# Performance work log

Measured on AMD Instinct MI355X. Metric: run time of the kernel, lower is better.

Reference implementation:

```python
import jax, jax.numpy as jnp
import numpy as np

AVG_LEN = 60.0
EPS = 1e-5
L, B, C, E = 48, 16, 128, 128
N_AGG = 15  # 5 + 10 * len(['sum'])


def setup_inputs() -> dict:
    key = jax.random.key(0)
    k0, k1, k2, k3 = jax.random.split(key, 4)
    T = jax.random.normal(k0, (L, L, B, C), jnp.float32)
    mask = jax.random.randint(k1, (L, L, B), 0, 2) > 0
    running_mean = jnp.zeros((C,), jnp.float32)
    running_var = jnp.ones((C,), jnp.float32)
    bn_weight = jnp.ones((C,), jnp.float32)
    bn_bias = jnp.zeros((C,), jnp.float32)
    w1 = jax.random.normal(k2, (C, E), jnp.float32) / np.sqrt(C).astype(np.float32)
    b1 = jnp.zeros((E,), jnp.float32)
    w2 = jax.random.normal(k3, (N_AGG * E, C), jnp.float32) / np.sqrt(N_AGG * E).astype(np.float32)
    b2 = jnp.zeros((C,), jnp.float32)
    return dict(T=T, mask=mask, running_mean=running_mean, running_var=running_var,
                bn_weight=bn_weight, bn_bias=bn_bias, w1=w1, b1=b1, w2=w2, b2=b2)


def reference(T, mask, running_mean, running_var, bn_weight, bn_bias, w1, b1, w2, b2):
    n = T.shape[0]
    # MaskedBatchNorm2d, eval mode (running stats)
    Tn = (T - running_mean) / jnp.sqrt(running_var + EPS) * bn_weight + bn_bias
    H = jax.nn.silu(Tn @ w1 + b1)                      # [L, L, B, E]
    eye = jnp.eye(n, dtype=bool)                       # [L, L]
    mf = mask[..., None].astype(H.dtype)               # [L, L, B, 1]
    mdf = (mask & eye[:, :, None])[..., None].astype(H.dtype)
    idx = jnp.arange(n)
    diag = H[idx, idx]                                 # [L, B, E]

    def dembed(x):  # [L, B, E] -> [L, L, B, E] with x on the (0,1)-diagonal
        return jnp.where(eye[:, :, None, None], x[:, None], jnp.zeros((), H.dtype))

    bc = lambda x: jnp.broadcast_to(x, H.shape)
    Hm = H * mf
    row_agg = jnp.sum(Hm, axis=0) / AVG_LEN            # [L, B, E]
    col_agg = jnp.sum(Hm, axis=1) / AVG_LEN            # [L, B, E]
    diag_agg = jnp.sum(H * mdf, axis=(0, 1)) / AVG_LEN # [B, E]
    all_agg = jnp.sum(Hm, axis=(0, 1)) / (AVG_LEN ** 2)  # [B, E]

    parts = [
        dembed(diag), bc(diag[None]), bc(diag[:, None]), jnp.swapaxes(H, 0, 1), H,
        dembed(row_agg), dembed(col_agg),
        dembed(jnp.broadcast_to(diag_agg[None], diag.shape)),
        bc(diag_agg[None, None]), bc(row_agg[None]), bc(col_agg[None]),
        bc(all_agg[None, None]), bc(col_agg[:, None]), bc(row_agg[:, None]),
        bc(all_agg[None, None]),
    ]
    outputs = jnp.concatenate(parts, axis=3)           # [L, L, B, 15*E]
    return outputs @ w2 + b2
```

## Files before the change

### kernel.cpp

```cpp
#include <hip/hip_runtime.h>

typedef __attribute__((ext_vector_type(8))) short short8;
typedef __attribute__((ext_vector_type(4))) float f32x4;
typedef __attribute__((ext_vector_type(4))) unsigned short ushort4_t;

#define NL 48
#define NB 16
#define NROWS (NL*NL*NB)

#define HB_N     (NROWS*128/2)
#define HB_OFF   0
#define W1T_OFF  (HB_OFF + HB_N)
#define W34T_OFF (W1T_OFF + 8192)
#define WD_OFF   (W34T_OFF + 16384)
#define X2_OFF   (WD_OFF + 73728)
#define VEC_N    (NL*NB*128)
#define RA_OFF   (X2_OFF + 147456)
#define AJ_OFF   (RA_OFF + VEC_N)
#define AI_OFF   (AJ_OFF + VEC_N)
#define AD_OFF   (AI_OFF + VEC_N)
#define AB_OFF   (AD_OFF + VEC_N)
#define DGA_OFF  (AB_OFF + NB*128)
#define FLAG_OFF (DGA_OFF + NB*128)

__device__ __forceinline__ float silu_f(float x) { return x / (1.0f + __expf(-x)); }
__device__ __forceinline__ unsigned short f2bf(float x) {
  union { float f; unsigned u; } v; v.f = x;
  unsigned r = v.u + 0x7fffu + ((v.u >> 16) & 1u);
  return (unsigned short)(r >> 16);
}
__device__ __forceinline__ float bf2f(unsigned short h) {
  union { unsigned u; float f; } v; v.u = ((unsigned)h) << 16; return v.f;
}

__global__ __launch_bounds__(256) void kPrep(const float* __restrict__ w1,
    const float* __restrict__ w2, const unsigned char* __restrict__ mb,
    unsigned short* __restrict__ w1t, unsigned short* __restrict__ w34t,
    unsigned short* __restrict__ wd, int* __restrict__ flag)
{
  __shared__ float t[64*65];
  __shared__ int any;
  int blk = blockIdx.x, tid = threadIdx.x;
  if (blk < 4) {
    int k0 = (blk & 1)*64, n0 = (blk >> 1)*64;
    #pragma unroll
    for (int it = 0; it < 16; ++it) { int f = it*256+tid; int kk=f>>6, nn=f&63;
      t[kk*65+nn] = w1[(k0+kk)*128 + n0+nn]; }
    __syncthreads();
    #pragma unroll
    for (int it = 0; it < 16; ++it) { int f = it*256+tid; int nn=f>>6, kk=f&63;
      w1t[(n0+nn)*128 + k0+kk] = f2bf(t[kk*65+nn]); }
  } else if (blk < 12) {
    int q = blk-4; int k0 = (q&3)*64, n0 = (q>>2)*64;
    #pragma unroll
    for (int it = 0; it < 16; ++it) { int f = it*256+tid; int kk=f>>6, nn=f&63;
      int k = k0+kk; int slice = (k < 128) ? 4 : 3;
      t[kk*65+nn] = w2[slice*16384 + (k&127)*128 + n0+nn]; }
    __syncthreads();
    #pragma unroll
    for (int it = 0; it < 16; ++it) { int f = it*256+tid; int nn=f>>6, kk=f&63;
      w34t[(n0+nn)*256 + k0+kk] = f2bf(t[kk*65+nn]); }
  } else if (blk < 48) {
    int q = blk-12; int k0 = (q%6)*64, n0 = (q/6)*64;
    int nq = n0 >> 7, kq = k0 >> 7;
    int slice;
    {
      const int sl_aj[3] = {1,9,10};
      const int sl_ai[3] = {2,13,12};
      const int sl_ad[3] = {0,5,6};
      slice = (nq==0) ? sl_aj[kq] : (nq==1) ? sl_ai[kq] : sl_ad[kq];
    }
    int nb = n0 & 127;
    #pragma unroll
    for (int it = 0; it < 16; ++it) { int f = it*256+tid; int kk=f>>6, nn=f&63;
      t[kk*65+nn] = w2[slice*16384 + ((k0&127)+kk)*128 + nb+nn]; }
    __syncthreads();
    #pragma unroll
    for (int it = 0; it < 16; ++it) { int f = it*256+tid; int nn=f>>6, kk=f&63;
      wd[(n0+nn)*384 + k0+kk] = f2bf(t[kk*65+nn]); }
  } else {
    if (tid == 0) any = 0;
    __syncthreads();
    int acc = 0;
    #pragma unroll
    for (int k2 = 0; k2 < 12; ++k2) {
      uchar4 v = ((const uchar4*)mb)[tid + k2*256];
      acc |= v.y | v.z | v.w;
    }
    if (acc) atomicOr(&any, 1);
    __syncthreads();
    if (tid == 0) *flag = any ? 1 : 4;
  }
}

__global__ __launch_bounds__(256) void kA(const float* __restrict__ T,
    const float* __restrict__ rmean, const float* __restrict__ rvar,
    const float* __restrict__ bw, const float* __restrict__ bb,
    const unsigned short* __restrict__ w1t, const float* __restrict__ b1,
    unsigned short* __restrict__ Hb)
{
  __shared__ __align__(16) char XDS[64*256];
  __shared__ __align__(16) char WDS[128*256];
  int tid = threadIdx.x;
  int m0 = blockIdx.x * 64;

  int cbase = (tid & 31) * 4;
  float scr[4], shr[4];
  #pragma unroll
  for (int u = 0; u < 4; ++u) {
    float s = bw[cbase+u] * rsqrtf(rvar[cbase+u] + 1e-5f);
    scr[u] = s; shr[u] = bb[cbase+u] - rmean[cbase+u] * s;
  }
  #pragma unroll
  for (int t = 0; t < 8; ++t) {
    int f = t*256 + tid;
    int r = f >> 5, c4 = f & 31;
    float4 v = *(const float4*)&T[(m0 + r)*128 + c4*4];
    ushort4_t p;
    p.x = f2bf(v.x*scr[0] + shr[0]); p.y = f2bf(v.y*scr[1] + shr[1]);
    p.z = f2bf(v.z*scr[2] + shr[2]); p.w = f2bf(v.w*scr[3] + shr[3]);
    *(ushort4_t*)(XDS + r*256 + ((c4*8) ^ ((r & 7) << 4))) = p;
  }
  #pragma unroll
  for (int t = 0; t < 8; ++t) {
    int f = t*256 + tid;
    int r = f >> 4, c16 = f & 15;
    short8 v = *(const short8*)(w1t + r*128 + c16*8);
    *(short8*)(WDS + r*256 + ((c16*16) ^ ((r & 7) << 4))) = v;
  }
  __syncthreads();

  int wave = tid >> 6, lane = tid & 63;
  int ln = lane & 15, lg = lane >> 4;
  int rw = (wave >> 1) * 32, cw = (wave & 1) * 64;
  int swz = (ln & 7) << 4;
  f32x4 acc[2][4];
  #pragma unroll
  for (int mt = 0; mt < 2; ++mt)
    #pragma unroll
    for (int nt = 0; nt < 4; ++nt) acc[mt][nt] = (f32x4){0.f,0.f,0.f,0.f};

  #pragma unroll
  for (int ks = 0; ks < 4; ++ks) {
    int kb = ks*64 + lg*16;
    short8 a[2], b[4];
    #pragma unroll
    for (int mt = 0; mt < 2; ++mt)
      a[mt] = *(const short8*)(XDS + (rw + mt*16 + ln)*256 + (kb ^ swz));
    #pragma unroll
    for (int nt = 0; nt < 4; ++nt)
      b[nt] = *(const short8*)(WDS + (cw + nt*16 + ln)*256 + (kb ^ swz));
    #pragma unroll
    for (int mt = 0; mt < 2; ++mt)
      #pragma unroll
      for (int nt = 0; nt < 4; ++nt)
        acc[mt][nt] = __builtin_amdgcn_mfma_f32_16x16x32_bf16(a[mt], b[nt], acc[mt][nt], 0, 0, 0);
  }
  float b1v[4];
  #pragma unroll
  for (int nt = 0; nt < 4; ++nt) b1v[nt] = b1[cw + nt*16 + ln];
  #pragma unroll
  for (int mt = 0; mt < 2; ++mt)
    #pragma unroll
    for (int q = 0; q < 4; ++q) {
      int m = m0 + rw + mt*16 + 4*lg + q;
      #pragma unroll
      for (int nt = 0; nt < 4; ++nt) {
        float x = acc[mt][nt][q] + b1v[nt];
        Hb[m*128 + cw + nt*16 + ln] = f2bf(silu_f(x));
      }
    }
}

__global__ __launch_bounds__(128) void kAgg(const unsigned short* __restrict__ Hb,
    const unsigned char* __restrict__ mb, const int* __restrict__ flag,
    float* __restrict__ ra, unsigned short* __restrict__ X2)
{
  int p = blockIdx.x, b = blockIdx.y;
  int tid = threadIdx.x;
  int s = *flag;
  int half = tid >> 6;
  int t = tid & 63;
  float a0 = 0.f, a1 = 0.f;
  #pragma unroll 16
  for (int q = 0; q < NL; ++q) {
    int mi = half ? ((q*NL + p)*NB + b) : ((p*NL + q)*NB + b);
    float mv = (float)mb[mi*s];
    unsigned u = *(const unsigned*)(Hb + mi*128 + 2*t);
    a0 += mv * bf2f((unsigned short)(u & 0xffffu));
    a1 += mv * bf2f((unsigned short)(u >> 16));
  }
  a0 *= (1.0f/60.0f); a1 *= (1.0f/60.0f);
  int ix = p*NB + b;
  unsigned pk = ((unsigned)f2bf(a1) << 16) | (unsigned)f2bf(a0);
  if (half) {
    *(float2*)(ra + ix*128 + 2*t) = make_float2(a0, a1);
    *(unsigned*)(X2 + ix*384 + 128 + 2*t) = pk;
  } else {
    *(unsigned*)(X2 + ix*384 + 256 + 2*t) = pk;
    unsigned d = *(const unsigned*)(Hb + ((p*NL + p)*NB + b)*128 + 2*t);
    *(unsigned*)(X2 + ix*384 + 2*t) = d;
  }
}

__global__ __launch_bounds__(256) void kDm(const unsigned short* __restrict__ X2,
    const unsigned short* __restrict__ wd,
    const unsigned short* __restrict__ Hb, const unsigned char* __restrict__ mb,
    const int* __restrict__ flag, const float* __restrict__ ra,
    const float* __restrict__ w2, const float* __restrict__ b2,
    float* __restrict__ Aj, float* __restrict__ Ai, float* __restrict__ Adg,
    float* __restrict__ Ab, float* __restrict__ Dga)
{
  int tid = threadIdx.x;
  if (blockIdx.y == 3) {
    int b = blockIdx.x;
    __shared__ float aas[128], dgs[128];
    int e = tid & 127;
    if (tid < 128) {
      int s = *flag;
      float aa = 0.f, dg = 0.f;
      #pragma unroll 8
      for (int p = 0; p < NL; ++p) {
        aa += ra[(p*NB + b)*128 + e];
        int mi = (p*NL + p)*NB + b;
        dg += (float)mb[mi*s] * bf2f(Hb[mi*128 + e]);
      }
      aas[e] = aa * (1.0f/60.0f);
      dgs[e] = dg * (1.0f/60.0f);
    }
    __syncthreads();
    if (tid < 128) {
      float ab = b2[e];
      #pragma unroll 8
      for (int k = 0; k < 128; ++k) {
        int o = k*128 + e;
        ab += dgs[k]*w2[8*16384 + o] + aas[k]*(w2[11*16384 + o] + w2[14*16384 + o]);
      }
      Ab[b*128 + e] = ab;
    } else {
      float dga = 0.f;
      #pragma unroll 8
      for (int k = 0; k < 128; ++k)
        dga += dgs[k]*w2[7*16384 + k*128 + e];
      Dga[b*128 + e] = dga;
    }
    return;
  }
  if (blockIdx.x >= 12) return;

  __shared__ __align__(16) char ADS[64*256];
  __shared__ __align__(16) char BDS[128*256];
  int m0 = blockIdx.x * 64;
  int n0 = blockIdx.y * 128;

  int wave = tid >> 6, lane = tid & 63;
  int ln = lane & 15, lg = lane >> 4;
  int rw = (wave >> 1) * 32, cw = (wave & 1) * 64;
  int swzk = (ln & 7) << 4;
  f32x4 acc[2][4];
  #pragma unroll
  for (int mt = 0; mt < 2; ++mt)
    #pragma unroll
    for (int nt = 0; nt < 4; ++nt) acc[mt][nt] = (f32x4){0.f,0.f,0.f,0.f};

  for (int kc = 0; kc < 3; ++kc) {
    if (kc) __syncthreads();
    #pragma unroll
    for (int t = 0; t < 4; ++t) {
      int f = t*256 + tid;
      int r = f >> 4, c16 = f & 15;
      short8 v = *(const short8*)(X2 + (m0 + r)*384 + kc*128 + c16*8);
      *(short8*)(ADS + r*256 + ((c16*16) ^ ((r & 7) << 4))) = v;
    }
    #pragma unroll
    for (int t = 0; t < 8; ++t) {
      int f = t*256 + tid;
      int r = f >> 4, c16 = f & 15;
      short8 v = *(const short8*)(wd + (n0 + r)*384 + kc*128 + c16*8);
      *(short8*)(BDS + r*256 + ((c16*16) ^ ((r & 7) << 4))) = v;
    }
    __syncthreads();
    #pragma unroll
    for (int ks = 0; ks < 4; ++ks) {
      int kb = ks*64 + lg*16;
      short8 a[2], b[4];
      #pragma unroll
      for (int mt = 0; mt < 2; ++mt)
        a[mt] = *(const short8*)(ADS + (rw + mt*16 + ln)*256 + (kb ^ swzk));
      #pragma unroll
      for (int nt = 0; nt < 4; ++nt)
        b[nt] = *(const short8*)(BDS + (cw + nt*16 + ln)*256 + (kb ^ swzk));
      #pragma unroll
      for (int mt = 0; mt < 2; ++mt)
        #pragma unroll
        for (int nt = 0; nt < 4; ++nt)
          acc[mt][nt] = __builtin_amdgcn_mfma_f32_16x16x32_bf16(a[mt], b[nt], acc[mt][nt], 0, 0, 0);
    }
  }
  float* outp = (blockIdx.y == 0) ? Aj : (blockIdx.y == 1) ? Ai : Adg;
  #pragma unroll
  for (int mt = 0; mt < 2; ++mt)
    #pragma unroll
    for (int q = 0; q < 4; ++q) {
      int row = m0 + rw + mt*16 + 4*lg + q;
      #pragma unroll
      for (int nt = 0; nt < 4; ++nt)
        outp[row*128 + cw + nt*16 + ln] = acc[mt][nt][q];
    }
}

__global__ __launch_bounds__(256) void kE(const unsigned short* __restrict__ Hb,
    const unsigned short* __restrict__ w34t,
    const float* __restrict__ Aj, const float* __restrict__ Ai,
    const float* __restrict__ Adg, const float* __restrict__ Ab,
    const float* __restrict__ Dga,
    float* __restrict__ out)
{
  __shared__ __align__(16) char ADS[64*512];
  __shared__ __align__(16) char BDS[128*256];
  int tid = threadIdx.x;
  int bi = blockIdx.x / 12;
  int j0 = (blockIdx.x % 12) * 4;

  #pragma unroll
  for (int t = 0; t < 8; ++t) {
    int f = t*256 + tid;
    int r = f >> 5, c16 = f & 31;
    int j = j0 + (r >> 4), b = r & 15;
    int srcrow = (c16 < 16) ? ((bi*NL + j)*NB + b) : ((j*NL + bi)*NB + b);
    short8 v = *(const short8*)(Hb + srcrow*128 + (c16 & 15)*8);
    *(short8*)(ADS + r*512 + ((c16*16) ^ ((r & 7) << 4))) = v;
  }

  int wave = tid >> 6, lane = tid & 63;
  int ln = lane & 15, lg = lane >> 4;
  int rw = (wave >> 1) * 32, cw = (wave & 1) * 64;
  int swz = (ln & 7) << 4;
  f32x4 acc[2][4];
  #pragma unroll
  for (int mt = 0; mt < 2; ++mt)
    #pragma unroll
    for (int nt = 0; nt < 4; ++nt) acc[mt][nt] = (f32x4){0.f,0.f,0.f,0.f};

  #pragma unroll
  for (int half = 0; half < 2; ++half) {
    __syncthreads();
    #pragma unroll
    for (int t = 0; t < 8; ++t) {
      int f = t*256 + tid;
      int r = f >> 4, c16 = f & 15;
      short8 v = *(const short8*)(w34t + r*256 + half*128 + c16*8);
      *(short8*)(BDS + r*256 + ((c16*16) ^ ((r & 7) << 4))) = v;
    }
    __syncthreads();
    #pragma unroll
    for (int ks = 0; ks < 4; ++ks) {
      int kbA = half*256 + ks*64 + lg*16;
      int kbB = ks*64 + lg*16;
      short8 a[2], b[4];
      #pragma unroll
      for (int mt = 0; mt < 2; ++mt)
        a[mt] = *(const short8*)(ADS + (rw + mt*16 + ln)*512 + (kbA ^ swz));
      #pragma unroll
      for (int nt = 0; nt < 4; ++nt)
        b[nt] = *(const short8*)(BDS + (cw + nt*16 + ln)*256 + (kbB ^ swz));
      #pragma unroll
      for (int mt = 0; mt < 2; ++mt)
        #pragma unroll
        for (int nt = 0; nt < 4; ++nt)
          acc[mt][nt] = __builtin_amdgcn_mfma_f32_16x16x32_bf16(a[mt], b[nt], acc[mt][nt], 0, 0, 0);
    }
  }

  #pragma unroll
  for (int mt = 0; mt < 2; ++mt) {
    int tb = rw + mt*16;
    int jj = tb >> 4;
    int j = j0 + jj;
    bool isdiag = (bi == j);
    #pragma unroll
    for (int q = 0; q < 4; ++q) {
      int b = 4*lg + q;
      int m = (bi*NL + j)*NB + b;
      #pragma unroll
      for (int nt = 0; nt < 4; ++nt) {
        int n = cw + nt*16 + ln;
        float add = Aj[(j*NB + b)*128 + n] + Ai[(bi*NB + b)*128 + n] + Ab[b*128 + n];
        if (isdiag) add += Adg[(bi*NB + b)*128 + n] + Dga[b*128 + n];
        out[m*128 + n] = acc[mt][nt][q] + add;
      }
    }
  }
}

extern "C" void kernel_launch(void* const* d_in, const int* in_sizes, int n_in,
                              void* d_out, int out_size, void* d_ws, size_t ws_size,
                              hipStream_t stream) {
  (void)in_sizes; (void)n_in; (void)out_size; (void)ws_size;
  const float* T      = (const float*)d_in[0];
  const unsigned char* mask = (const unsigned char*)d_in[1];
  const float* rmean  = (const float*)d_in[2];
  const float* rvar   = (const float*)d_in[3];
  const float* bw     = (const float*)d_in[4];
  const float* bb     = (const float*)d_in[5];
  const float* w1     = (const float*)d_in[6];
  const float* b1     = (const float*)d_in[7];
  const float* w2     = (const float*)d_in[8];
  const float* b2     = (const float*)d_in[9];
  float* ws  = (float*)d_ws;
  float* out = (float*)d_out;

  unsigned short* Hb   = (unsigned short*)(ws + HB_OFF);
  unsigned short* w1t  = (unsigned short*)(ws + W1T_OFF);
  unsigned short* w34t = (unsigned short*)(ws + W34T_OFF);
  unsigned short* wd   = (unsigned short*)(ws + WD_OFF);
  unsigned short* X2   = (unsigned short*)(ws + X2_OFF);
  float* ra   = ws + RA_OFF;
  float* Aj   = ws + AJ_OFF;
  float* Ai   = ws + AI_OFF;
  float* Adg  = ws + AD_OFF;
  float* Ab   = ws + AB_OFF;
  float* Dga  = ws + DGA_OFF;
  int*   flag = (int*)(ws + FLAG_OFF);

  kPrep<<<49, 256, 0, stream>>>(w1, w2, mask, w1t, w34t, wd, flag);
  kA<<<NROWS/64, 256, 0, stream>>>(T, rmean, rvar, bw, bb, w1t, b1, Hb);
  kAgg<<<dim3(NL, NB), 128, 0, stream>>>(Hb, mask, flag, ra, X2);
  kDm<<<dim3(16, 4), 256, 0, stream>>>(X2, wd, Hb, mask, flag, ra, w2, b2, Aj, Ai, Adg, Ab, Dga);
  kE<<<NROWS/64, 256, 0, stream>>>(Hb, w34t, Aj, Ai, Adg, Ab, Dga, out);
}
```

Before: 59.91 us.

## Fold weight prep into first GEMM kernel and halve kE A-tile LDS

Removes the separate kPrep launch. Its w2 transposes and the mask-flag computation now run in extra blocks appended to kA's grid, and each kA block converts and transposes w1 into LDS itself. kE now loads its A tile per half (Hb row, then the transposed row) into a 64x256-byte buffer, which halves its LDS footprint and allows more occupancy. The trade-off is that w1 is redundantly read from fp32 with strided loads in all 576 kA blocks, and the kE A loads now sit behind a barrier inside the loop.

```diff
diff --git a/kernel.cpp b/kernel.cpp
--- a/kernel.cpp
+++ b/kernel.cpp
@@ -10,8 +10,7 @@
 
 #define HB_N     (NROWS*128/2)
 #define HB_OFF   0
-#define W1T_OFF  (HB_OFF + HB_N)
-#define W34T_OFF (W1T_OFF + 8192)
+#define W34T_OFF (HB_OFF + HB_N)
 #define WD_OFF   (W34T_OFF + 16384)
 #define X2_OFF   (WD_OFF + 73728)
 #define VEC_N    (NL*NB*128)
@@ -33,77 +32,69 @@
   union { unsigned u; float f; } v; v.u = ((unsigned)h) << 16; return v.f;
 }
 
-__global__ __launch_bounds__(256) void kPrep(const float* __restrict__ w1,
-    const float* __restrict__ w2, const unsigned char* __restrict__ mb,
-    unsigned short* __restrict__ w1t, unsigned short* __restrict__ w34t,
-    unsigned short* __restrict__ wd, int* __restrict__ flag)
-{
-  __shared__ float t[64*65];
-  __shared__ int any;
-  int blk = blockIdx.x, tid = threadIdx.x;
-  if (blk < 4) {
-    int k0 = (blk & 1)*64, n0 = (blk >> 1)*64;
-    #pragma unroll
-    for (int it = 0; it < 16; ++it) { int f = it*256+tid; int kk=f>>6, nn=f&63;
-      t[kk*65+nn] = w1[(k0+kk)*128 + n0+nn]; }
-    __syncthreads();
-    #pragma unroll
-    for (int it = 0; it < 16; ++it) { int f = it*256+tid; int nn=f>>6, kk=f&63;
-      w1t[(n0+nn)*128 + k0+kk] = f2bf(t[kk*65+nn]); }
-  } else if (blk < 12) {
-    int q = blk-4; int k0 = (q&3)*64, n0 = (q>>2)*64;
-    #pragma unroll
-    for (int it = 0; it < 16; ++it) { int f = it*256+tid; int kk=f>>6, nn=f&63;
-      int k = k0+kk; int slice = (k < 128) ? 4 : 3;
-      t[kk*65+nn] = w2[slice*16384 + (k&127)*128 + n0+nn]; }
-    __syncthreads();
-    #pragma unroll
-    for (int it = 0; it < 16; ++it) { int f = it*256+tid; int nn=f>>6, kk=f&63;
-      w34t[(n0+nn)*256 + k0+kk] = f2bf(t[kk*65+nn]); }
-  } else if (blk < 48) {
-    int q = blk-12; int k0 = (q%6)*64, n0 = (q/6)*64;
-    int nq = n0 >> 7, kq = k0 >> 7;
-    int slice;
-    {
-      const int sl_aj[3] = {1,9,10};
-      const int sl_ai[3] = {2,13,12};
-      const int sl_ad[3] = {0,5,6};
-      slice = (nq==0) ? sl_aj[kq] : (nq==1) ? sl_ai[kq] : sl_ad[kq];
-    }
-    int nb = n0 & 127;
-    #pragma unroll
-    for (int it = 0; it < 16; ++it) { int f = it*256+tid; int kk=f>>6, nn=f&63;
-      t[kk*65+nn] = w2[slice*16384 + ((k0&127)+kk)*128 + nb+nn]; }
-    __syncthreads();
-    #pragma unroll
-    for (int it = 0; it < 16; ++it) { int f = it*256+tid; int nn=f>>6, kk=f&63;
-      wd[(n0+nn)*384 + k0+kk] = f2bf(t[kk*65+nn]); }
-  } else {
-    if (tid == 0) any = 0;
-    __syncthreads();
-    int acc = 0;
-    #pragma unroll
-    for (int k2 = 0; k2 < 12; ++k2) {
-      uchar4 v = ((const uchar4*)mb)[tid + k2*256];
-      acc |= v.y | v.z | v.w;
-    }
-    if (acc) atomicOr(&any, 1);
-    __syncthreads();
-    if (tid == 0) *flag = any ? 1 : 4;
-  }
-}
-
 __global__ __launch_bounds__(256) void kA(const float* __restrict__ T,
     const float* __restrict__ rmean, const float* __restrict__ rvar,
     const float* __restrict__ bw, const float* __restrict__ bb,
-    const unsigned short* __restrict__ w1t, const float* __restrict__ b1,
-    unsigned short* __restrict__ Hb)
+    const float* __restrict__ w1, const float* __restrict__ b1,
+    const float* __restrict__ w2, const unsigned char* __restrict__ mb,
+    unsigned short* __restrict__ Hb, unsigned short* __restrict__ w34t,
+    unsigned short* __restrict__ wd, int* __restrict__ flag)
 {
-  __shared__ __align__(16) char XDS[64*256];
-  __shared__ __align__(16) char WDS[128*256];
+  __shared__ __align__(16) char SM[49152];
+  __shared__ int any;
+  char* XDS = SM;
+  char* WDS = SM + 16384;
+  float* tt = (float*)SM;
   int tid = threadIdx.x;
-  int m0 = blockIdx.x * 64;
-
+  int blk = blockIdx.x;
+
+  if (blk >= 576) {
+    int pb = blk - 576;
+    if (pb < 8) {
+      int k0 = (pb & 3)*64, n0 = (pb >> 2)*64;
+      #pragma unroll
+      for (int it = 0; it < 16; ++it) { int f = it*256+tid; int kk=f>>6, nn=f&63;
+        int k = k0+kk; int slice = (k < 128) ? 4 : 3;
+        tt[kk*65+nn] = w2[slice*16384 + (k&127)*128 + n0+nn]; }
+      __syncthreads();
+      #pragma unroll
+      for (int it = 0; it < 16; ++it) { int f = it*256+tid; int nn=f>>6, kk=f&63;
+        w34t[(n0+nn)*256 + k0+kk] = f2bf(tt[kk*65+nn]); }
+    } else if (pb < 44) {
+      int q = pb-8; int k0 = (q%6)*64, n0 = (q/6)*64;
+      int nq = n0 >> 7, kq = k0 >> 7;
+      int slice;
+      {
+        const int sl_aj[3] = {1,9,10};
+        const int sl_ai[3] = {2,13,12};
+        const int sl_ad[3] = {0,5,6};
+        slice = (nq==0) ? sl_aj[kq] : (nq==1) ? sl_ai[kq] : sl_ad[kq];
+      }
+      int nb = n0 & 127;
+      #pragma unroll
+      for (int it = 0; it < 16; ++it) { int f = it*256+tid; int kk=f>>6, nn=f&63;
+        tt[kk*65+nn] = w2[slice*16384 + ((k0&127)+kk)*128 + nb+nn]; }
+      __syncthreads();
+      #pragma unroll
+      for (int it = 0; it < 16; ++it) { int f = it*256+tid; int nn=f>>6, kk=f&63;
+        wd[(n0+nn)*384 + k0+kk] = f2bf(tt[kk*65+nn]); }
+    } else {
+      if (tid == 0) any = 0;
+      __syncthreads();
+      int acc = 0;
+      #pragma unroll
+      for (int k2 = 0; k2 < 12; ++k2) {
+        uchar4 v = ((const uchar4*)mb)[tid + k2*256];
+        acc |= v.y | v.z | v.w;
+      }
+      if (acc) atomicOr(&any, 1);
+      __syncthreads();
+      if (tid == 0) *flag = any ? 1 : 4;
+    }
+    return;
+  }
+
+  int m0 = blk * 64;
   int cbase = (tid & 31) * 4;
   float scr[4], shr[4];
   #pragma unroll
@@ -121,12 +112,17 @@
     p.z = f2bf(v.z*scr[2] + shr[2]); p.w = f2bf(v.w*scr[3] + shr[3]);
     *(ushort4_t*)(XDS + r*256 + ((c4*8) ^ ((r & 7) << 4))) = p;
   }
-  #pragma unroll
-  for (int t = 0; t < 8; ++t) {
-    int f = t*256 + tid;
-    int r = f >> 4, c16 = f & 15;
-    short8 v = *(const short8*)(w1t + r*128 + c16*8);
-    *(short8*)(WDS + r*256 + ((c16*16) ^ ((r & 7) << 4))) = v;
+  {
+    int n = tid & 127, ch = (tid >> 7) * 8;
+    #pragma unroll
+    for (int cc = 0; cc < 8; ++cc) {
+      int c = ch + cc;
+      short8 v;
+      #pragma unroll
+      for (int j = 0; j < 8; ++j)
+        ((unsigned short*)&v)[j] = f2bf(w1[(c*8 + j)*128 + n]);
+      *(short8*)(WDS + n*256 + ((c*16) ^ ((n & 7) << 4))) = v;
+    }
   }
   __syncthreads();
 
@@ -316,21 +312,12 @@
     const float* __restrict__ Dga,
     float* __restrict__ out)
 {
-  __shared__ __align__(16) char ADS[64*512];
+  __shared__ __align__(16) char ADS[64*256];
   __shared__ __align__(16) char BDS[128*256];
   int tid = threadIdx.x;
   int bi = blockIdx.x / 12;
   int j0 = (blockIdx.x % 12) * 4;
-
-  #pragma unroll
-  for (int t = 0; t < 8; ++t) {
-    int f = t*256 + tid;
-    int r = f >> 5, c16 = f & 31;
-    int j = j0 + (r >> 4), b = r & 15;
-    int srcrow = (c16 < 16) ? ((bi*NL + j)*NB + b) : ((j*NL + bi)*NB + b);
-    short8 v = *(const short8*)(Hb + srcrow*128 + (c16 & 15)*8);
-    *(short8*)(ADS + r*512 + ((c16*16) ^ ((r & 7) << 4))) = v;
-  }
+  int m0 = (bi*NL + j0) * NB;
 
   int wave = tid >> 6, lane = tid & 63;
   int ln = lane & 15, lg = lane >> 4;
@@ -344,7 +331,15 @@
 
   #pragma unroll
   for (int half = 0; half < 2; ++half) {
-    __syncthreads();
+    if (half) __syncthreads();
+    #pragma unroll
+    for (int t = 0; t < 4; ++t) {
+      int f = t*256 + tid;
+      int r = f >> 4, c16 = f & 15;
+      int srcrow = (half == 0) ? (m0 + r) : ((j0 + (r >> 4))*NL + bi)*NB + (r & 15);
+      short8 v = *(const short8*)(Hb + srcrow*128 + c16*8);
+      *(short8*)(ADS + r*256 + ((c16*16) ^ ((r & 7) << 4))) = v;
+    }
     #pragma unroll
     for (int t = 0; t < 8; ++t) {
       int f = t*256 + tid;
@@ -355,15 +350,14 @@
     __syncthreads();
     #pragma unroll
     for (int ks = 0; ks < 4; ++ks) {
-      int kbA = half*256 + ks*64 + lg*16;
-      int kbB = ks*64 + lg*16;
+      int kb = ks*64 + lg*16;
       short8 a[2], b[4];
       #pragma unroll
       for (int mt = 0; mt < 2; ++mt)
-        a[mt] = *(const short8*)(ADS + (rw + mt*16 + ln)*512 + (kbA ^ swz));
+        a[mt] = *(const short8*)(ADS + (rw + mt*16 + ln)*256 + (kb ^ swz));
       #pragma unroll
       for (int nt = 0; nt < 4; ++nt)
-        b[nt] = *(const short8*)(BDS + (cw + nt*16 + ln)*256 + (kbB ^ swz));
+        b[nt] = *(const short8*)(BDS + (cw + nt*16 + ln)*256 + (kb ^ swz));
       #pragma unroll
       for (int mt = 0; mt < 2; ++mt)
         #pragma unroll
@@ -411,7 +405,6 @@
   float* out = (float*)d_out;
 
   unsigned short* Hb   = (unsigned short*)(ws + HB_OFF);
-  unsigned short* w1t  = (unsigned short*)(ws + W1T_OFF);
   unsigned short* w34t = (unsigned short*)(ws + W34T_OFF);
   unsigned short* wd   = (unsigned short*)(ws + WD_OFF);
   unsigned short* X2   = (unsigned short*)(ws + X2_OFF);
@@ -423,9 +416,10 @@
   float* Dga  = ws + DGA_OFF;
   int*   flag = (int*)(ws + FLAG_OFF);
 
-  kPrep<<<49, 256, 0, stream>>>(w1, w2, mask, w1t, w34t, wd, flag);
-  kA<<<NROWS/64, 256, 0, stream>>>(T, rmean, rvar, bw, bb, w1t, b1, Hb);
+  kA<<<621, 256, 0, stream>>>(T, rmean, rvar, bw, bb, w1, b1, w2, mask,
+                              Hb, w34t, wd, flag);
   kAgg<<<dim3(NL, NB), 128, 0, stream>>>(Hb, mask, flag, ra, X2);
-  kDm<<<dim3(16, 4), 256, 0, stream>>>(X2, wd, Hb, mask, flag, ra, w2, b2, Aj, Ai, Adg, Ab, Dga);
+  kDm<<<dim3(16, 4), 256, 0, stream>>>(X2, wd, Hb, mask, flag, ra, w2, b2,
+                                       Aj, Ai, Adg, Ab, Dga);
   kE<<<NROWS/64, 256, 0, stream>>>(Hb, w34t, Aj, Ai, Adg, Ab, Dga, out);
 }
```

Measured after the change: 50.42 us. 15.8% less time.
